# Kernel tuning notes

Measured on AMD Instinct MI355X. Metric: run time of the kernel, lower is better.

Reference implementation:

```python
import jax, jax.numpy as jnp
import numpy as np

EPS = 1e-8  # torch.cosine_similarity default eps

def setup_inputs() -> dict:
    key = jax.random.key(0)
    k1, k2 = jax.random.split(key)
    embeddings = jax.random.normal(k1, (2048, 4096), dtype=jnp.float32)
    table = jax.random.normal(k2, (50257, 4096), dtype=jnp.float32)
    return {"embeddings": embeddings, "table": table}

def reference(embeddings, table):
    # cosine_similarity(x, y) = (x . y) / (max(||x||, eps) * max(||y||, eps))
    # Normalize each side first, then a single [P,D]x[D,V] GEMM -> [P,V];
    # avoids materializing the [P,V,D] broadcast intermediate.
    e_norm = jnp.maximum(jnp.linalg.norm(embeddings, axis=-1, keepdims=True), EPS)
    t_norm = jnp.maximum(jnp.linalg.norm(table, axis=-1, keepdims=True), EPS)
    e = embeddings / e_norm            # [P, D]
    t = table / t_norm                 # [V, D]
    sims = jnp.einsum('pd,vd->pv', e, t)  # [P, V]
    ids = jnp.argmax(sims, axis=-1)    # [P]
    return ids
```

## Files before the change

### kernel.cpp

```cpp
#include <hip/hip_runtime.h>
#include <hip/hip_bf16.h>
#include <stdint.h>

#define P 2048
#define V 50257
#define D 4096
#define CAP 128
#define MARGIN 1.5e-3f

#define BM 128
#define BN 128
#define BK 32

using frag_ab = __attribute__((ext_vector_type(8))) short;
using frag_cd = __attribute__((ext_vector_type(4))) float;

__device__ __forceinline__ unsigned short f2bf(float f) {
    __hip_bfloat16 h = __float2bfloat16(f);
    return *(unsigned short*)&h;
}

__device__ __forceinline__ uint32_t fkey(float f) {
    uint32_t u = __float_as_uint(f);
    return (u & 0x80000000u) ? ~u : (u | 0x80000000u);
}
__device__ __forceinline__ float key2f(uint32_t k) {
    uint32_t u = (k & 0x80000000u) ? (k ^ 0x80000000u) : ~k;
    return __uint_as_float(u);
}

#define GLD_LDS16(g, l) __builtin_amdgcn_global_load_lds(                      \
    (const __attribute__((address_space(1))) void*)(g),                        \
    (__attribute__((address_space(3))) void*)(l), 16, 0, 0)

__global__ __launch_bounds__(256) void normalize_e(
        const float* __restrict__ E, unsigned short* __restrict__ Abf,
        unsigned long long* __restrict__ packmax, int* __restrict__ cnt) {
    const int p = blockIdx.x;
    const int t = threadIdx.x;
    const float* row = E + (size_t)p * D;

    float4 vals[4];
    float ss = 0.f;
#pragma unroll
    for (int c = 0; c < 4; c++) {
        vals[c] = ((const float4*)row)[c * 256 + t];
        ss += vals[c].x * vals[c].x + vals[c].y * vals[c].y
            + vals[c].z * vals[c].z + vals[c].w * vals[c].w;
    }
#pragma unroll
    for (int o = 1; o < 64; o <<= 1) ss += __shfl_xor(ss, o);
    __shared__ float wss[4];
    if ((t & 63) == 0) wss[t >> 6] = ss;
    __syncthreads();
    float tot = wss[0] + wss[1] + wss[2] + wss[3];
    float inv = 1.0f / fmaxf(sqrtf(tot), 1e-8f);

    unsigned short* dst = Abf + (size_t)p * D;
#pragma unroll
    for (int c = 0; c < 4; c++) {
        float4 v = vals[c];
        uint2 st;
        st.x = (uint32_t)f2bf(v.x * inv) | ((uint32_t)f2bf(v.y * inv) << 16);
        st.y = (uint32_t)f2bf(v.z * inv) | ((uint32_t)f2bf(v.w * inv) << 16);
        ((uint2*)dst)[c * 256 + t] = st;
    }
    if (t == 0) { packmax[p] = 0ull; cnt[p] = 0; }
}

__global__ __launch_bounds__(256) void normalize_t(
        const float* __restrict__ T, unsigned short* __restrict__ Tbf) {
    const int v = blockIdx.x;
    const int t = threadIdx.x;
    const float* row = T + (size_t)v * D;

    float4 vals[4];
    float ss = 0.f;
#pragma unroll
    for (int c = 0; c < 4; c++) {
        vals[c] = ((const float4*)row)[c * 256 + t];
        ss += vals[c].x * vals[c].x + vals[c].y * vals[c].y
            + vals[c].z * vals[c].z + vals[c].w * vals[c].w;
    }
#pragma unroll
    for (int o = 1; o < 64; o <<= 1) ss += __shfl_xor(ss, o);
    __shared__ float wss[4];
    if ((t & 63) == 0) wss[t >> 6] = ss;
    __syncthreads();
    float tot = wss[0] + wss[1] + wss[2] + wss[3];
    float inv = 1.0f / fmaxf(sqrtf(tot), 1e-8f);

    unsigned short* dst = Tbf + (size_t)v * D;
#pragma unroll
    for (int c = 0; c < 4; c++) {
        float4 x = vals[c];
        uint2 st;
        st.x = (uint32_t)f2bf(x.x * inv) | ((uint32_t)f2bf(x.y * inv) << 16);
        st.y = (uint32_t)f2bf(x.z * inv) | ((uint32_t)f2bf(x.w * inv) << 16);
        ((uint2*)dst)[c * 256 + t] = st;
    }
}

__global__ __launch_bounds__(256) void gemm_bf16_argmax(
        const unsigned short* __restrict__ Abf,
        const unsigned short* __restrict__ Tbf,
        unsigned long long* __restrict__ packmax,
        int* __restrict__ cnt, int* __restrict__ cand) {
    __shared__ unsigned short As[BM * BK];
    __shared__ unsigned short Bs[BN * BK];

    const int t = threadIdx.x;
    const int m0 = blockIdx.x * BM;
    const int v0 = blockIdx.y * BN;
    const int lane = t & 63;
    const int w = t >> 6;
    const int wm = w & 1, wn = w >> 1;
    const int l15 = lane & 15, lq = lane >> 4;

    const int srow = lane >> 2;
    const int scol = (lane & 3) * 8;
    const unsigned short* gA0 = Abf + (size_t)(m0 + w * 16 + srow) * D + scol;
    const unsigned short* gA1 = gA0 + (size_t)64 * D;
    int rb0 = v0 + w * 16 + srow;      if (rb0 > V - 1) rb0 = V - 1;
    int rb1 = v0 + (w + 4) * 16 + srow; if (rb1 > V - 1) rb1 = V - 1;
    const unsigned short* gB0 = Tbf + (size_t)rb0 * D + scol;
    const unsigned short* gB1 = Tbf + (size_t)rb1 * D + scol;
    unsigned short* lA0 = &As[(size_t)w * 512];
    unsigned short* lA1 = &As[(size_t)(w + 4) * 512];
    unsigned short* lB0 = &Bs[(size_t)w * 512];
    unsigned short* lB1 = &Bs[(size_t)(w + 4) * 512];

    frag_cd acc[4][4] = {};

    for (int k0 = 0; k0 < D; k0 += BK) {
        __syncthreads();
        GLD_LDS16(gA0 + k0, lA0);
        GLD_LDS16(gA1 + k0, lA1);
        GLD_LDS16(gB0 + k0, lB0);
        GLD_LDS16(gB1 + k0, lB1);
        __syncthreads();

        frag_ab af[4], bf[4];
#pragma unroll
        for (int i = 0; i < 4; i++)
            af[i] = *(const frag_ab*)&As[(wm * 64 + i * 16 + l15) * BK + lq * 8];
#pragma unroll
        for (int j = 0; j < 4; j++)
            bf[j] = *(const frag_ab*)&Bs[(wn * 64 + j * 16 + l15) * BK + lq * 8];
#pragma unroll
        for (int i = 0; i < 4; i++)
#pragma unroll
            for (int j = 0; j < 4; j++)
                acc[i][j] = __builtin_amdgcn_mfma_f32_16x16x32_bf16(af[i], bf[j], acc[i][j], 0, 0, 0);
    }

#pragma unroll
    for (int i = 0; i < 4; i++) {
#pragma unroll
        for (int r = 0; r < 4; r++) {
            const int p = m0 + wm * 64 + i * 16 + lq * 4 + r;
            float sc[4];
            int nidx[4];
            unsigned long long best = 0ull;
#pragma unroll
            for (int j = 0; j < 4; j++) {
                int nl = wn * 64 + j * 16 + l15;
                int n = v0 + nl;
                float s = -2.0f;
                if (n < V) s = acc[i][j][r];
                sc[j] = s; nidx[j] = n;
                if (n < V) {
                    unsigned long long pk =
                        ((unsigned long long)fkey(s) << 32) |
                        (unsigned long long)(0xFFFFFFFFu - (uint32_t)n);
                    if (pk > best) best = pk;
                }
            }
#pragma unroll
            for (int o = 1; o < 16; o <<= 1) {
                unsigned long long other = __shfl_xor(best, o);
                if (other > best) best = other;
            }
            unsigned long long oldpk = 0ull;
            if (l15 == 0) oldpk = atomicMax(packmax + p, best);
            oldpk = __shfl(oldpk, lane & 48);
            unsigned long long merged = best > oldpk ? best : oldpk;
            float thr = key2f((uint32_t)(merged >> 32)) - MARGIN;
#pragma unroll
            for (int j = 0; j < 4; j++) {
                if (nidx[j] < V && sc[j] >= thr) {
                    int slot = atomicAdd(cnt + p, 1);
                    if (slot < CAP) cand[p * CAP + slot] = nidx[j];
                }
            }
        }
    }
}

__global__ __launch_bounds__(256) void gemm_argmax(
        const unsigned short* __restrict__ Abf,
        const float* __restrict__ T,
        unsigned long long* __restrict__ packmax,
        int* __restrict__ cnt, int* __restrict__ cand) {
    __shared__ unsigned short As[BM * BK];
    __shared__ unsigned short Bs[BN * BK];
    __shared__ float invt[BN];

    const int t = threadIdx.x;
    const int m0 = blockIdx.x * BM;
    const int v0 = blockIdx.y * BN;
    const int lane = t & 63;
    const int wm = (t >> 6) & 1, wn = (t >> 6) >> 1;
    const int l15 = lane & 15, lq = lane >> 4;
    const int r0 = t >> 2, q0 = t & 3;

    frag_cd acc[4][4] = {};
    float ssq0 = 0.f, ssq1 = 0.f;

    for (int k0 = 0; k0 < D; k0 += BK) {
        uint4 areg[2];
        float4 b0[2], b1[2];
#pragma unroll
        for (int pass = 0; pass < 2; pass++) {
            int row = pass * 64 + r0;
            areg[pass] = *(const uint4*)(Abf + (size_t)(m0 + row) * D + k0 + q0 * 8);
            int v = v0 + row;
            if (v < V) {
                const float* src = T + (size_t)v * D + k0 + q0 * 8;
                b0[pass] = *(const float4*)src;
                b1[pass] = *(const float4*)(src + 4);
            } else {
                b0[pass] = float4{0.f, 0.f, 0.f, 0.f};
                b1[pass] = float4{0.f, 0.f, 0.f, 0.f};
            }
        }
        __syncthreads();
#pragma unroll
        for (int pass = 0; pass < 2; pass++) {
            *(uint4*)&As[(size_t)(pass * 256 + t) * 8] = areg[pass];
            float4 x = b0[pass], y = b1[pass];
            float s = x.x * x.x + x.y * x.y + x.z * x.z + x.w * x.w
                    + y.x * y.x + y.y * y.y + y.z * y.z + y.w * y.w;
            if (pass == 0) ssq0 += s; else ssq1 += s;
            uint4 bv;
            bv.x = (uint32_t)f2bf(x.x) | ((uint32_t)f2bf(x.y) << 16);
            bv.y = (uint32_t)f2bf(x.z) | ((uint32_t)f2bf(x.w) << 16);
            bv.z = (uint32_t)f2bf(y.x) | ((uint32_t)f2bf(y.y) << 16);
            bv.w = (uint32_t)f2bf(y.z) | ((uint32_t)f2bf(y.w) << 16);
            *(uint4*)&Bs[(size_t)(pass * 256 + t) * 8] = bv;
        }
        __syncthreads();

        frag_ab af[4], bf[4];
#pragma unroll
        for (int i = 0; i < 4; i++)
            af[i] = *(const frag_ab*)&As[(wm * 64 + i * 16 + l15) * BK + lq * 8];
#pragma unroll
        for (int j = 0; j < 4; j++)
            bf[j] = *(const frag_ab*)&Bs[(wn * 64 + j * 16 + l15) * BK + lq * 8];
#pragma unroll
        for (int i = 0; i < 4; i++)
#pragma unroll
            for (int j = 0; j < 4; j++)
                acc[i][j] = __builtin_amdgcn_mfma_f32_16x16x32_bf16(af[i], bf[j], acc[i][j], 0, 0, 0);
    }

    ssq0 += __shfl_xor(ssq0, 1); ssq0 += __shfl_xor(ssq0, 2);
    ssq1 += __shfl_xor(ssq1, 1); ssq1 += __shfl_xor(ssq1, 2);
    __syncthreads();
    if ((t & 3) == 0) {
        invt[r0]      = ssq0 > 0.f ? rsqrtf(ssq0) : 0.f;
        invt[64 + r0] = ssq1 > 0.f ? rsqrtf(ssq1) : 0.f;
    }
    __syncthreads();

#pragma unroll
    for (int i = 0; i < 4; i++) {
#pragma unroll
        for (int r = 0; r < 4; r++) {
            const int p = m0 + wm * 64 + i * 16 + lq * 4 + r;
            float sc[4];
            int nidx[4];
            unsigned long long best = 0ull;
#pragma unroll
            for (int j = 0; j < 4; j++) {
                int nl = wn * 64 + j * 16 + l15;
                int n = v0 + nl;
                float s = -2.0f;
                if (n < V) s = acc[i][j][r] * invt[nl];
                sc[j] = s; nidx[j] = n;
                if (n < V) {
                    unsigned long long pk =
                        ((unsigned long long)fkey(s) << 32) |
                        (unsigned long long)(0xFFFFFFFFu - (uint32_t)n);
                    if (pk > best) best = pk;
                }
            }
#pragma unroll
            for (int o = 1; o < 16; o <<= 1) {
                unsigned long long other = __shfl_xor(best, o);
                if (other > best) best = other;
            }
            unsigned long long oldpk = 0ull;
            if (l15 == 0) oldpk = atomicMax(packmax + p, best);
            oldpk = __shfl(oldpk, lane & 48);
            unsigned long long merged = best > oldpk ? best : oldpk;
            float thr = key2f((uint32_t)(merged >> 32)) - MARGIN;
#pragma unroll
            for (int j = 0; j < 4; j++) {
                if (nidx[j] < V && sc[j] >= thr) {
                    int slot = atomicAdd(cnt + p, 1);
                    if (slot < CAP) cand[p * CAP + slot] = nidx[j];
                }
            }
        }
    }
}

__global__ __launch_bounds__(256) void rescore(
        const float* __restrict__ E, const float* __restrict__ T,
        const unsigned long long* __restrict__ packmax,
        const int* __restrict__ cnt, const int* __restrict__ cand,
        int* __restrict__ out) {
    const int p = blockIdx.x;
    const int t = threadIdx.x;
    const int w = t >> 6, lane = t & 63;
    const float* e = E + (size_t)p * D;

    const int c = cnt[p];
    const bool overflow = c > CAP;
    const int ncand = overflow ? 0 : c;

    unsigned long long pk = packmax[p];
    const int pv = (int)(0xFFFFFFFFu - (uint32_t)(pk & 0xFFFFFFFFull));

    double best_s = -3.0;
    int best_v = 0x7FFFFFFF;

    auto evalw = [&](int v) -> double {
        const float* tr = T + (size_t)v * D;
        double dot = 0.0, ss = 0.0;
        for (int i = lane; i < D; i += 64) {
            double ev = e[i], tv = tr[i];
            dot += ev * tv;
            ss  += tv * tv;
        }
#pragma unroll
        for (int o = 1; o < 64; o <<= 1) {
            dot += __shfl_xor(dot, o);
            ss  += __shfl_xor(ss, o);
        }
        return dot / fmax(sqrt(ss), 1e-8);
    };
    auto consider = [&](int v, double s) {
        if (s > best_s || (s == best_s && v < best_v)) { best_s = s; best_v = v; }
    };

    if (!overflow) {
        const int total = ncand + 1;
        for (int idx = w; idx < total; idx += 4) {
            int v = (idx == 0) ? pv : cand[p * CAP + idx - 1];
            consider(v, evalw(v));
        }
    } else {
        for (int v = w; v < V; v += 4) consider(v, evalw(v));
    }

    __shared__ double bs[4];
    __shared__ int bv[4];
    if (lane == 0) { bs[w] = best_s; bv[w] = best_v; }
    __syncthreads();
    if (t == 0) {
        double s = bs[0]; int v = bv[0];
#pragma unroll
        for (int i = 1; i < 4; i++)
            if (bs[i] > s || (bs[i] == s && bv[i] < v)) { s = bs[i]; v = bv[i]; }
        out[p] = v;
    }
}

extern "C" void kernel_launch(void* const* d_in, const int* in_sizes, int n_in,
                              void* d_out, int out_size, void* d_ws, size_t ws_size,
                              hipStream_t stream) {
    const float* E = (const float*)d_in[0];
    const float* T = (const float*)d_in[1];
    int* out = (int*)d_out;

    char* ws = (char*)d_ws;

    const size_t FAST_WS = 429555712ull;

    if (ws_size >= FAST_WS) {
        unsigned short* Tbf = (unsigned short*)ws;
        unsigned short* Abf = (unsigned short*)(ws + 411705344ull);
        unsigned long long* packmax = (unsigned long long*)(ws + 428482560ull);
        int* cnt  = (int*)(ws + 428498944ull);
        int* cand = (int*)(ws + 428507136ull);

        normalize_e<<<P, 256, 0, stream>>>(E, Abf, packmax, cnt);
        normalize_t<<<V, 256, 0, stream>>>(T, Tbf);
        dim3 g1(P / BM, (V + BN - 1) / BN);
        gemm_bf16_argmax<<<g1, 256, 0, stream>>>(Abf, Tbf, packmax, cnt, cand);
        rescore<<<P, 256, 0, stream>>>(E, T, packmax, cnt, cand, out);
    } else {
        unsigned short* Abf = (unsigned short*)ws;
        unsigned long long* packmax = (unsigned long long*)(ws + 16777216);
        int* cnt  = (int*)(ws + 16793600);
        int* cand = (int*)(ws + 16801792);

        normalize_e<<<P, 256, 0, stream>>>(E, Abf, packmax, cnt);
        dim3 g1(P / BM, (V + BN - 1) / BN);
        gemm_argmax<<<g1, 256, 0, stream>>>(Abf, T, packmax, cnt, cand);
        rescore<<<P, 256, 0, stream>>>(E, T, packmax, cnt, cand, out);
    }
}
```

Measured before the change: 2.416 ms.

## Switch candidate-screening GEMM from bf16 to scaled FP8 e4m3 MFMA

Normalized embeddings and table rows are now quantized to FP8 e4m3 (scaled by 256) instead of bf16, and the screening GEMM uses the 16x16x128 f8f6f4 scaled MFMA with a 128-wide K tile and XOR-swizzled LDS layout. This halves the bytes written by normalization and read by the GEMM, and doubles the K per MFMA instruction. To absorb the larger quantization error, the candidate margin is raised and the candidate cap quadrupled, which increases work in the fp32 rescore pass and raises the chance of overflowing the candidate list.

```diff
diff --git a/kernel.cpp b/kernel.cpp
--- a/kernel.cpp
+++ b/kernel.cpp
@@ -5,21 +5,40 @@
 #define P 2048
 #define V 50257
 #define D 4096
-#define CAP 128
-#define MARGIN 1.5e-3f
+#define CAP 512
+#define MARGIN 1.0e-2f
 
 #define BM 128
 #define BN 128
 #define BK 32
+#define BKF 128
 
 using frag_ab = __attribute__((ext_vector_type(8))) short;
 using frag_cd = __attribute__((ext_vector_type(4))) float;
+using i32x4   = __attribute__((ext_vector_type(4))) int;
+using i32x8   = __attribute__((ext_vector_type(8))) int;
 
 __device__ __forceinline__ unsigned short f2bf(float f) {
     __hip_bfloat16 h = __float2bfloat16(f);
     return *(unsigned short*)&h;
 }
 
+__device__ __forceinline__ unsigned char f2e4m3(float f) {
+    uint32_t u = __float_as_uint(f);
+    unsigned char sign = (unsigned char)((u >> 24) & 0x80u);
+    uint32_t a = u & 0x7FFFFFFFu;
+    if (a >= 0x43E00000u) return sign | 0x7E;
+    if (a < 0x3C800000u) {
+        float af = __uint_as_float(a);
+        int q = __float2int_rn(af * 512.0f);
+        return sign | (unsigned char)q;
+    }
+    uint32_t r = a + 0x0007FFFFu + ((a >> 20) & 1u);
+    int eb = (int)(r >> 23) - 127 + 7;
+    uint32_t m = (r >> 20) & 7u;
+    return sign | (unsigned char)((eb << 3) | m);
+}
+
 __device__ __forceinline__ uint32_t fkey(float f) {
     uint32_t u = __float_as_uint(f);
     return (u & 0x80000000u) ? ~u : (u | 0x80000000u);
@@ -33,8 +52,8 @@
     (const __attribute__((address_space(1))) void*)(g),                        \
     (__attribute__((address_space(3))) void*)(l), 16, 0, 0)
 
-__global__ __launch_bounds__(256) void normalize_e(
-        const float* __restrict__ E, unsigned short* __restrict__ Abf,
+__global__ __launch_bounds__(256) void normalize_e8(
+        const float* __restrict__ E, unsigned char* __restrict__ A8,
         unsigned long long* __restrict__ packmax, int* __restrict__ cnt) {
     const int p = blockIdx.x;
     const int t = threadIdx.x;
@@ -54,22 +73,23 @@
     if ((t & 63) == 0) wss[t >> 6] = ss;
     __syncthreads();
     float tot = wss[0] + wss[1] + wss[2] + wss[3];
-    float inv = 1.0f / fmaxf(sqrtf(tot), 1e-8f);
-
-    unsigned short* dst = Abf + (size_t)p * D;
+    float s = 256.0f / fmaxf(sqrtf(tot), 1e-8f);
+
+    unsigned char* dst = A8 + (size_t)p * D;
 #pragma unroll
     for (int c = 0; c < 4; c++) {
         float4 v = vals[c];
-        uint2 st;
-        st.x = (uint32_t)f2bf(v.x * inv) | ((uint32_t)f2bf(v.y * inv) << 16);
-        st.y = (uint32_t)f2bf(v.z * inv) | ((uint32_t)f2bf(v.w * inv) << 16);
-        ((uint2*)dst)[c * 256 + t] = st;
+        uint32_t b = (uint32_t)f2e4m3(v.x * s)
+                   | ((uint32_t)f2e4m3(v.y * s) << 8)
+                   | ((uint32_t)f2e4m3(v.z * s) << 16)
+                   | ((uint32_t)f2e4m3(v.w * s) << 24);
+        ((uint32_t*)dst)[c * 256 + t] = b;
     }
     if (t == 0) { packmax[p] = 0ull; cnt[p] = 0; }
 }
 
-__global__ __launch_bounds__(256) void normalize_t(
-        const float* __restrict__ T, unsigned short* __restrict__ Tbf) {
+__global__ __launch_bounds__(256) void normalize_t8(
+        const float* __restrict__ T, unsigned char* __restrict__ T8) {
     const int v = blockIdx.x;
     const int t = threadIdx.x;
     const float* row = T + (size_t)v * D;
@@ -88,26 +108,27 @@
     if ((t & 63) == 0) wss[t >> 6] = ss;
     __syncthreads();
     float tot = wss[0] + wss[1] + wss[2] + wss[3];
-    float inv = 1.0f / fmaxf(sqrtf(tot), 1e-8f);
-
-    unsigned short* dst = Tbf + (size_t)v * D;
+    float s = 256.0f / fmaxf(sqrtf(tot), 1e-8f);
+
+    unsigned char* dst = T8 + (size_t)v * D;
 #pragma unroll
     for (int c = 0; c < 4; c++) {
         float4 x = vals[c];
-        uint2 st;
-        st.x = (uint32_t)f2bf(x.x * inv) | ((uint32_t)f2bf(x.y * inv) << 16);
-        st.y = (uint32_t)f2bf(x.z * inv) | ((uint32_t)f2bf(x.w * inv) << 16);
-        ((uint2*)dst)[c * 256 + t] = st;
-    }
-}
-
-__global__ __launch_bounds__(256) void gemm_bf16_argmax(
-        const unsigned short* __restrict__ Abf,
-        const unsigned short* __restrict__ Tbf,
+        uint32_t b = (uint32_t)f2e4m3(x.x * s)
+                   | ((uint32_t)f2e4m3(x.y * s) << 8)
+                   | ((uint32_t)f2e4m3(x.z * s) << 16)
+                   | ((uint32_t)f2e4m3(x.w * s) << 24);
+        ((uint32_t*)dst)[c * 256 + t] = b;
+    }
+}
+
+__global__ __launch_bounds__(256) void gemm_fp8_argmax(
+        const unsigned char* __restrict__ A8,
+        const unsigned char* __restrict__ T8,
         unsigned long long* __restrict__ packmax,
         int* __restrict__ cnt, int* __restrict__ cand) {
-    __shared__ unsigned short As[BM * BK];
-    __shared__ unsigned short Bs[BN * BK];
+    __shared__ __align__(16) unsigned char As[BM * BKF];
+    __shared__ __align__(16) unsigned char Bs[BN * BKF];
 
     const int t = threadIdx.x;
     const int m0 = blockIdx.x * BM;
@@ -117,41 +138,58 @@
     const int wm = w & 1, wn = w >> 1;
     const int l15 = lane & 15, lq = lane >> 4;
 
-    const int srow = lane >> 2;
-    const int scol = (lane & 3) * 8;
-    const unsigned short* gA0 = Abf + (size_t)(m0 + w * 16 + srow) * D + scol;
-    const unsigned short* gA1 = gA0 + (size_t)64 * D;
-    int rb0 = v0 + w * 16 + srow;      if (rb0 > V - 1) rb0 = V - 1;
-    int rb1 = v0 + (w + 4) * 16 + srow; if (rb1 > V - 1) rb1 = V - 1;
-    const unsigned short* gB0 = Tbf + (size_t)rb0 * D + scol;
-    const unsigned short* gB1 = Tbf + (size_t)rb1 * D + scol;
-    unsigned short* lA0 = &As[(size_t)w * 512];
-    unsigned short* lA1 = &As[(size_t)(w + 4) * 512];
-    unsigned short* lB0 = &Bs[(size_t)w * 512];
-    unsigned short* lB1 = &Bs[(size_t)(w + 4) * 512];
+    const int sr = lane >> 3;
+    const int sj = (lane & 7) ^ sr;
+    const unsigned char* gA = A8 + (size_t)(m0 + w * 32 + sr) * D + sj * 16;
+    const unsigned char* gB[4];
+#pragma unroll
+    for (int g = 0; g < 4; g++) {
+        int r = v0 + w * 32 + g * 8 + sr;
+        if (r > V - 1) r = V - 1;
+        gB[g] = T8 + (size_t)r * D + sj * 16;
+    }
+    unsigned char* lA = As + w * 4096;
+    unsigned char* lB = Bs + w * 4096;
 
     frag_cd acc[4][4] = {};
 
-    for (int k0 = 0; k0 < D; k0 += BK) {
+    for (int k0 = 0; k0 < D; k0 += BKF) {
         __syncthreads();
-        GLD_LDS16(gA0 + k0, lA0);
-        GLD_LDS16(gA1 + k0, lA1);
-        GLD_LDS16(gB0 + k0, lB0);
-        GLD_LDS16(gB1 + k0, lB1);
+#pragma unroll
+        for (int g = 0; g < 4; g++) {
+            GLD_LDS16(gA + (size_t)g * 8 * D + k0, lA + g * 1024);
+            GLD_LDS16(gB[g] + k0, lB + g * 1024);
+        }
         __syncthreads();
 
-        frag_ab af[4], bf[4];
+        i32x8 af[4], bfr[4];
+#pragma unroll
+        for (int i = 0; i < 4; i++) {
+            const int row = wm * 64 + i * 16 + l15;
+            const int sw = (row & 7) << 4;
+            const int base = row * BKF;
+            i32x4 h0 = *(const i32x4*)&As[base + ((lq * 32) ^ sw)];
+            i32x4 h1 = *(const i32x4*)&As[base + ((lq * 32 + 16) ^ sw)];
+            af[i] = __builtin_shufflevector(h0, h1, 0, 1, 2, 3, 4, 5, 6, 7);
+        }
+#pragma unroll
+        for (int j = 0; j < 4; j++) {
+            const int row = wn * 64 + j * 16 + l15;
+            const int sw = (row & 7) << 4;
+            const int base = row * BKF;
+            i32x4 h0 = *(const i32x4*)&Bs[base + ((lq * 32) ^ sw)];
+            i32x4 h1 = *(const i32x4*)&Bs[base + ((lq * 32 + 16) ^ sw)];
+            bfr[j] = __builtin_shufflevector(h0, h1, 0, 1, 2, 3, 4, 5, 6, 7);
+        }
 #pragma unroll
         for (int i = 0; i < 4; i++)
-            af[i] = *(const frag_ab*)&As[(wm * 64 + i * 16 + l15) * BK + lq * 8];
-#pragma unroll
-        for (int j = 0; j < 4; j++)
-            bf[j] = *(const frag_ab*)&Bs[(wn * 64 + j * 16 + l15) * BK + lq * 8];
-#pragma unroll
-        for (int i = 0; i < 4; i++)
 #pragma unroll
             for (int j = 0; j < 4; j++)
-                acc[i][j] = __builtin_amdgcn_mfma_f32_16x16x32_bf16(af[i], bf[j], acc[i][j], 0, 0, 0);
+                acc[i][j] = __builtin_amdgcn_mfma_scale_f32_16x16x128_f8f6f4(
+                    af[i], bfr[j], acc[i][j],
+                    0, 0,
+                    0, 0x7F7F7F7F,
+                    0, 0x7F7F7F7F);
     }
 
 #pragma unroll
@@ -167,7 +205,7 @@
                 int nl = wn * 64 + j * 16 + l15;
                 int n = v0 + nl;
                 float s = -2.0f;
-                if (n < V) s = acc[i][j][r];
+                if (n < V) s = acc[i][j][r] * 0x1p-16f;
                 sc[j] = s; nidx[j] = n;
                 if (n < V) {
                     unsigned long long pk =
@@ -195,6 +233,41 @@
             }
         }
     }
+}
+
+__global__ __launch_bounds__(256) void normalize_e(
+        const float* __restrict__ E, unsigned short* __restrict__ Abf,
+        unsigned long long* __restrict__ packmax, int* __restrict__ cnt) {
+    const int p = blockIdx.x;
+    const int t = threadIdx.x;
+    const float* row = E + (size_t)p * D;
+
+    float4 vals[4];
+    float ss = 0.f;
+#pragma unroll
+    for (int c = 0; c < 4; c++) {
+        vals[c] = ((const float4*)row)[c * 256 + t];
+        ss += vals[c].x * vals[c].x + vals[c].y * vals[c].y
+            + vals[c].z * vals[c].z + vals[c].w * vals[c].w;
+    }
+#pragma unroll
+    for (int o = 1; o < 64; o <<= 1) ss += __shfl_xor(ss, o);
+    __shared__ float wss[4];
+    if ((t & 63) == 0) wss[t >> 6] = ss;
+    __syncthreads();
+    float tot = wss[0] + wss[1] + wss[2] + wss[3];
+    float inv = 1.0f / fmaxf(sqrtf(tot), 1e-8f);
+
+    unsigned short* dst = Abf + (size_t)p * D;
+#pragma unroll
+    for (int c = 0; c < 4; c++) {
+        float4 v = vals[c];
+        uint2 st;
+        st.x = (uint32_t)f2bf(v.x * inv) | ((uint32_t)f2bf(v.y * inv) << 16);
+        st.y = (uint32_t)f2bf(v.z * inv) | ((uint32_t)f2bf(v.w * inv) << 16);
+        ((uint2*)dst)[c * 256 + t] = st;
+    }
+    if (t == 0) { packmax[p] = 0ull; cnt[p] = 0; }
 }
 
 __global__ __launch_bounds__(256) void gemm_argmax(
@@ -388,19 +461,19 @@
 
     char* ws = (char*)d_ws;
 
-    const size_t FAST_WS = 429555712ull;
+    const size_t FAST_WS = 218460160ull;
 
     if (ws_size >= FAST_WS) {
-        unsigned short* Tbf = (unsigned short*)ws;
-        unsigned short* Abf = (unsigned short*)(ws + 411705344ull);
-        unsigned long long* packmax = (unsigned long long*)(ws + 428482560ull);
-        int* cnt  = (int*)(ws + 428498944ull);
-        int* cand = (int*)(ws + 428507136ull);
-
-        normalize_e<<<P, 256, 0, stream>>>(E, Abf, packmax, cnt);
-        normalize_t<<<V, 256, 0, stream>>>(T, Tbf);
+        unsigned char* T8 = (unsigned char*)ws;
+        unsigned char* A8 = (unsigned char*)(ws + 205852672ull);
+        unsigned long long* packmax = (unsigned long long*)(ws + 214241280ull);
+        int* cnt  = (int*)(ws + 214257664ull);
+        int* cand = (int*)(ws + 214265856ull);
+
+        normalize_e8<<<P, 256, 0, stream>>>(E, A8, packmax, cnt);
+        normalize_t8<<<V, 256, 0, stream>>>(T, T8);
         dim3 g1(P / BM, (V + BN - 1) / BN);
-        gemm_bf16_argmax<<<g1, 256, 0, stream>>>(Abf, Tbf, packmax, cnt, cand);
+        gemm_fp8_argmax<<<g1, 256, 0, stream>>>(A8, T8, packmax, cnt, cand);
         rescore<<<P, 256, 0, stream>>>(E, T, packmax, cnt, cand, out);
     } else {
         unsigned short* Abf = (unsigned short*)ws;
```

After: 2.935 ms. +21.5%, slower.
